# Performance work log

Measured on AMD Instinct MI355X. Metric: run time of the kernel, lower is better.

The kernel has to match this reference:

```python
import jax, jax.numpy as jnp
import numpy as np

N_NODES = 10000
W_DIM = 512
N_EDGES = 200000


def setup_inputs() -> dict:
    key = jax.random.key(0)
    k1, k2, k3 = jax.random.split(key, 3)
    z_drug = jax.random.normal(k1, (N_NODES, W_DIM), dtype=jnp.float32)
    # glorot-style init for the bilinear weight
    glorot_std = jnp.sqrt(2.0 / (W_DIM + W_DIM)).astype(jnp.float32)
    weight = jax.random.normal(k2, (W_DIM, W_DIM), dtype=jnp.float32) * glorot_std
    batch_edges = jax.random.randint(k3, (2, N_EDGES), 0, N_NODES, dtype=jnp.int64)
    return {"z_drug": z_drug, "weight": weight, "batch_edges": batch_edges}


def reference(z_drug, weight, batch_edges):
    # edge_type == 'drug_drug': both endpoints come from the drug table.
    row_embed = z_drug[batch_edges[0]]  # [E, d]
    col_embed = z_drug[batch_edges[1]]  # [E, d]
    # score_e = row_e @ W @ col_e  == diag((Z1 W) Z2^T) without the N x N blowup
    score = jnp.einsum('ed,df,ef->e', row_embed, weight, col_embed)
    return jax.nn.sigmoid(score)  # is_sigmoid=True default
```

## Files before the change

### kernel.cpp

```cpp
#include <hip/hip_runtime.h>
#include <math.h>

#define DIM     512
#define NNODES  10000
#define NEDGES  200000
#define MPAD    10240
#define NMB     160
#define GEMM_GRID (NMB * 4)
#define BKT     157

#define HIST_BLK   64
#define SCAN_BID   64
#define SCAT_BASE  65
#define SCAT_N     199
#define GEMM_BASE  264
#define FUSE_GRID  (GEMM_BASE + GEMM_GRID)
#define ECHUNK     25000

using floatx4 = __attribute__((ext_vector_type(4))) float;
using half8   = __attribute__((ext_vector_type(8))) _Float16;
using half2v  = __attribute__((ext_vector_type(2))) _Float16;
typedef unsigned long long ull;

template <int N> struct IC { static constexpr int v = N; };

__device__ inline float dot2acc(half2v a, half2v b, float c) {
#if __has_builtin(__builtin_amdgcn_fdot2)
    return __builtin_amdgcn_fdot2(a, b, c, false);
#else
    return fmaf((float)a[0], (float)b[0], fmaf((float)a[1], (float)b[1], c));
#endif
}

__device__ inline int aload(const int* p) {
    return __hip_atomic_load(p, __ATOMIC_RELAXED, __HIP_MEMORY_SCOPE_AGENT);
}
__device__ inline void astore(int* p, int v) {
    __hip_atomic_store(p, v, __ATOMIC_RELAXED, __HIP_MEMORY_SCOPE_AGENT);
}
__device__ inline void waitflag(int* f, int target) {
    while (__hip_atomic_load(f, __ATOMIC_RELAXED, __HIP_MEMORY_SCOPE_AGENT) < target)
        __builtin_amdgcn_s_sleep(8);
    __atomic_signal_fence(__ATOMIC_ACQUIRE);
}
__device__ inline void signal(int* f) {
    __atomic_signal_fence(__ATOMIC_RELEASE);
    __hip_atomic_fetch_add(f, 1, __ATOMIC_RELAXED, __HIP_MEMORY_SCOPE_AGENT);
}

#define PREP_ZBLK 2560
#define PREP_GRID (PREP_ZBLK + 64)
__global__ __launch_bounds__(256) void prep(const float* __restrict__ Z,
                                            const float* __restrict__ W,
                                            _Float16* __restrict__ Zh16,
                                            _Float16* __restrict__ Wh16t,
                                            int* __restrict__ counts) {
    const int b = blockIdx.x;
    const int t = threadIdx.x;

    if (b == 0 && t < BKT + 4) counts[t] = 0;

    if (b < PREP_ZBLK) {
        const int idx8 = (b * 256 + t) * 8;
        const int m = idx8 >> 9;
        float x[8];
        if (m < NNODES) {
            float4 v0 = *(const float4*)(Z + idx8);
            float4 v1 = *(const float4*)(Z + idx8 + 4);
            x[0]=v0.x; x[1]=v0.y; x[2]=v0.z; x[3]=v0.w;
            x[4]=v1.x; x[5]=v1.y; x[6]=v1.z; x[7]=v1.w;
        } else {
            #pragma unroll
            for (int j = 0; j < 8; ++j) x[j] = 0.f;
        }
        half8 h;
        #pragma unroll
        for (int j = 0; j < 8; ++j) h[j] = (_Float16)x[j];
        *(half8*)(Zh16 + idx8) = h;
    } else {
        __shared__ float tile[64][65];
        const int wb = b - PREP_ZBLK;
        const int kb = (wb >> 3) * 64;
        const int nb = (wb & 7) * 64;
        const int kk = t >> 2;
        const int ch = t & 3;

        const float* src = W + (size_t)(kb + kk) * DIM + nb + ch * 16;
        #pragma unroll
        for (int q = 0; q < 4; ++q) {
            float4 v = *(const float4*)(src + q * 4);
            tile[kk][ch * 16 + q * 4 + 0] = v.x;
            tile[kk][ch * 16 + q * 4 + 1] = v.y;
            tile[kk][ch * 16 + q * 4 + 2] = v.z;
            tile[kk][ch * 16 + q * 4 + 3] = v.w;
        }
        __syncthreads();

        const int nn = kk;
        half8 h0, h1;
        #pragma unroll
        for (int i = 0; i < 8; ++i) h0[i] = (_Float16)tile[ch * 16 + i][nn];
        #pragma unroll
        for (int i = 0; i < 8; ++i) h1[i] = (_Float16)tile[ch * 16 + 8 + i][nn];
        _Float16* d = Wh16t + (size_t)(nb + nn) * DIM + kb + ch * 16;
        *(half8*)(d)     = h0;
        *(half8*)(d + 8) = h1;
    }
}

__global__ __launch_bounds__(256, 3) void gemm_sort(
        const _Float16* __restrict__ Zh16,
        const _Float16* __restrict__ Wh16t,
        _Float16* __restrict__ ZWh,
        const int* __restrict__ eidx,
        int* __restrict__ counts,
        int* __restrict__ cursor,
        ull* __restrict__ slots,
        int* __restrict__ flags)
{
    __shared__ _Float16 Abuf[2][2 * 64 * 32];
    __shared__ _Float16 Bbuf[2][2 * 128 * 32];
    __shared__ int s_cnt[BKT], s_base[BKT], s_off[BKT];
    __shared__ int s_scan[256];

    const int t   = threadIdx.x;
    const int bid = blockIdx.x;

    if (bid >= GEMM_BASE) {
        const int s8  = bid - GEMM_BASE;
        const int cxd = bid & 7;
        const int rr  = s8 >> 3;
        const int mg  = (rr >> 2) * 8 + cxd;
        const int m0  = mg * 64;
        const int n0  = (rr & 3) * 128;

        const int l  = t & 63;
        const int w  = t >> 6;
        const int wn = w * 32;
        const int lm = l & 15;
        const int lq = l >> 4;
        const unsigned wbase = (unsigned)(t & 192);

        floatx4 acc[4][2] = {};

        auto stage = [&](int buf, int k0) {
            #pragma unroll
            for (int p = 0; p < 2; ++p) {
                const int s   = p * 256 + t;
                const int kk  = s >> 8;
                const int row = (s >> 2) & 63;
                const int ch  = s & 3;
                const _Float16* src = Zh16 + (size_t)(m0 + row) * DIM + k0 + kk * 32 + ch * 8;
                __builtin_amdgcn_global_load_lds(
                    (const __attribute__((address_space(1))) void*)src,
                    (__attribute__((address_space(3))) void*)&Abuf[buf][(p * 256 + wbase) * 8],
                    16, 0, 0);
            }
            #pragma unroll
            for (int p = 0; p < 4; ++p) {
                const int s   = p * 256 + t;
                const int kk  = s >> 9;
                const int row = (s >> 2) & 127;
                const int ch  = s & 3;
                const _Float16* src = Wh16t + (size_t)(n0 + row) * DIM + k0 + kk * 32 + ch * 8;
                __builtin_amdgcn_global_load_lds(
                    (const __attribute__((address_space(1))) void*)src,
                    (__attribute__((address_space(3))) void*)&Bbuf[buf][(p * 256 + wbase) * 8],
                    16, 0, 0);
            }
        };

        stage(0, 0);
        stage(1, 64);

        auto step = [&](auto Sc) {
            constexpr int S   = decltype(Sc)::v;
            constexpr int buf = S & 1;
            if constexpr (S < 7) asm volatile("s_waitcnt vmcnt(6)" ::: "memory");
            else                 asm volatile("s_waitcnt vmcnt(0)" ::: "memory");
            __builtin_amdgcn_sched_barrier(0);
            __builtin_amdgcn_s_barrier();
            __builtin_amdgcn_sched_barrier(0);

            half8 aF[2][4], bF[2][2];
            #pragma unroll
            for (int kk = 0; kk < 2; ++kk) {
                #pragma unroll
                for (int i = 0; i < 4; ++i)
                    aF[kk][i] = *(const half8*)&Abuf[buf][kk * 2048 + (16 * i + lm) * 32 + lq * 8];
                #pragma unroll
                for (int j = 0; j < 2; ++j)
                    bF[kk][j] = *(const half8*)&Bbuf[buf][kk * 4096 + (wn + 16 * j + lm) * 32 + lq * 8];
            }
            asm volatile("s_waitcnt lgkmcnt(0)" ::: "memory");
            __builtin_amdgcn_sched_barrier(0);
            __builtin_amdgcn_s_barrier();
            __builtin_amdgcn_sched_barrier(0);

            if constexpr (S < 6) stage(buf, (S + 2) * 64);

            #pragma unroll
            for (int kk = 0; kk < 2; ++kk)
                #pragma unroll
                for (int i = 0; i < 4; ++i)
                    #pragma unroll
                    for (int j = 0; j < 2; ++j)
                        acc[i][j] = __builtin_amdgcn_mfma_f32_16x16x32_f16(
                            aF[kk][i], bF[kk][j], acc[i][j], 0, 0, 0);
        };

        step(IC<0>{}); step(IC<1>{}); step(IC<2>{}); step(IC<3>{});
        step(IC<4>{}); step(IC<5>{}); step(IC<6>{}); step(IC<7>{});

        #pragma unroll
        for (int i = 0; i < 4; ++i)
            #pragma unroll
            for (int j = 0; j < 2; ++j)
                #pragma unroll
                for (int r = 0; r < 4; ++r) {
                    const int gm = m0 + 16 * i + lq * 4 + r;
                    const int gn = n0 + wn + 16 * j + lm;
                    if (gm < NNODES)
                        ZWh[(size_t)gm * DIM + gn] = (_Float16)acc[i][j][r];
                }
        return;
    }

    if (bid < HIST_BLK) {
        for (int i = t; i < BKT; i += 256) s_cnt[i] = 0;
        __syncthreads();
        for (int e = bid * 256 + t; e < NEDGES; e += HIST_BLK * 256)
            atomicAdd(&s_cnt[eidx[NEDGES + e] >> 6], 1);
        __syncthreads();
        for (int i = t; i < BKT; i += 256)
            if (s_cnt[i]) atomicAdd(&counts[i], s_cnt[i]);
        __syncthreads();
        if (t == 0) signal(&flags[0]);
        return;
    }

    if (bid == SCAN_BID) {
        if (t == 0) waitflag(&flags[0], HIST_BLK);
        __syncthreads();
        int v = (t < BKT) ? aload(counts + t) : 0;
        s_scan[t] = v;
        __syncthreads();
        #pragma unroll
        for (int off = 1; off < 256; off <<= 1) {
            int u = (t >= off) ? s_scan[t - off] : 0;
            __syncthreads();
            s_scan[t] += u;
            __syncthreads();
        }
        if (t < BKT) astore(cursor + t, s_scan[t] - v);
        __syncthreads();
        if (t == 0) signal(&flags[1]);
        return;
    }

    {
        const int sb = bid - SCAT_BASE;
        for (int i = t; i < BKT; i += 256) { s_cnt[i] = 0; s_off[i] = 0; }
        __syncthreads();
        const int e0 = sb * 1024;
        int myb[4];
        #pragma unroll
        for (int q = 0; q < 4; ++q) {
            int e = e0 + q * 256 + t;
            if (e < NEDGES) { myb[q] = eidx[NEDGES + e] >> 6; atomicAdd(&s_cnt[myb[q]], 1); }
            else myb[q] = -1;
        }
        __syncthreads();
        if (t == 0) waitflag(&flags[1], 1);
        __syncthreads();
        for (int i = t; i < BKT; i += 256)
            if (s_cnt[i]) s_base[i] = atomicAdd(&cursor[i], s_cnt[i]);
        __syncthreads();
        #pragma unroll
        for (int q = 0; q < 4; ++q)
            if (myb[q] >= 0) {
                int e = e0 + q * 256 + t;
                int r = eidx[e];
                int c = eidx[NEDGES + e];
                int pos = s_base[myb[q]] + atomicAdd(&s_off[myb[q]], 1);
                slots[pos] = ((ull)(unsigned)r << 32) |
                             (ull)(((unsigned)c << 18) | (unsigned)e);
            }
    }
}

__global__ __launch_bounds__(256) void edge_score_b(const _Float16* __restrict__ ZWh,
                                                    const _Float16* __restrict__ Zh,
                                                    const ull* __restrict__ slots,
                                                    float* __restrict__ out) {
    const int t    = threadIdx.x;
    const int lane = t & 63;
    const int gq   = lane >> 4;
    const int sl   = lane & 15;

    const int chunk = blockIdx.x & 7;
    const int blk   = blockIdx.x >> 3;
    const int ii    = chunk * ECHUNK + blk * 16 + (t >> 6) * 4 + gq;
    if (ii >= (chunk + 1) * ECHUNK) return;

    const ull  v = slots[ii];
    const unsigned k = (unsigned)v;
    const int c = (int)(k >> 18);
    const int r = (int)((v >> 32) & 0xFFFFu);

    const _Float16* rp = ZWh + (size_t)r * DIM + sl * 32;
    const _Float16* cp = Zh  + (size_t)c * DIM + sl * 32;

    half8 ra0 = *(const half8*)(rp);
    half8 ra1 = *(const half8*)(rp + 8);
    half8 ra2 = *(const half8*)(rp + 16);
    half8 ra3 = *(const half8*)(rp + 24);
    half8 c0  = *(const half8*)(cp);
    half8 c1  = *(const half8*)(cp + 8);
    half8 c2  = *(const half8*)(cp + 16);
    half8 c3  = *(const half8*)(cp + 24);

    float s = 0.f;
    #pragma unroll
    for (int d = 0; d < 4; ++d) {
        s = dot2acc((half2v){ra0[2*d], ra0[2*d+1]}, (half2v){c0[2*d], c0[2*d+1]}, s);
        s = dot2acc((half2v){ra1[2*d], ra1[2*d+1]}, (half2v){c1[2*d], c1[2*d+1]}, s);
        s = dot2acc((half2v){ra2[2*d], ra2[2*d+1]}, (half2v){c2[2*d], c2[2*d+1]}, s);
        s = dot2acc((half2v){ra3[2*d], ra3[2*d+1]}, (half2v){c3[2*d], c3[2*d+1]}, s);
    }

    s += __shfl_xor(s, 1, 64);
    s += __shfl_xor(s, 2, 64);
    s += __shfl_xor(s, 4, 64);
    s += __shfl_xor(s, 8, 64);

    if (sl == 0)
        out[k & 0x3FFFFu] = 1.0f / (1.0f + expf(-s));
}

#define GTM 128
#define GTN 64
#define GTK 16
#define LDA 132
#define LDB 68

__global__ __launch_bounds__(256) void gemm_zw(const float* __restrict__ A,
                                               const float* __restrict__ B,
                                               float* __restrict__ C) {
    __shared__ float As[GTK * LDA];
    __shared__ float Bs[GTK * LDB];

    const int t  = threadIdx.x;
    const int m0 = blockIdx.x * GTM;
    const int n0 = blockIdx.y * GTN;
    const int tx = t & 15;
    const int ty = t >> 4;

    float acc[8][4] = {};

    for (int k0 = 0; k0 < DIM; k0 += GTK) {
        #pragma unroll
        for (int p = 0; p < 2; ++p) {
            int f  = t + p * 256;
            int mm = f >> 2;
            int kq = f & 3;
            int m  = m0 + mm;
            float4 v = make_float4(0.f, 0.f, 0.f, 0.f);
            if (m < NNODES)
                v = *(const float4*)(A + (size_t)m * DIM + k0 + kq * 4);
            As[(kq * 4 + 0) * LDA + mm] = v.x;
            As[(kq * 4 + 1) * LDA + mm] = v.y;
            As[(kq * 4 + 2) * LDA + mm] = v.z;
            As[(kq * 4 + 3) * LDA + mm] = v.w;
        }
        {
            int kb = t >> 4, n4 = t & 15;
            *(float4*)&Bs[kb * LDB + n4 * 4] =
                *(const float4*)(B + (size_t)(k0 + kb) * DIM + n0 + n4 * 4);
        }
        __syncthreads();

        #pragma unroll
        for (int kk = 0; kk < GTK; ++kk) {
            float4 a0 = *(const float4*)&As[kk * LDA + ty * 8];
            float4 a1 = *(const float4*)&As[kk * LDA + ty * 8 + 4];
            float4 b  = *(const float4*)&Bs[kk * LDB + tx * 4];
            float av[8] = {a0.x, a0.y, a0.z, a0.w, a1.x, a1.y, a1.z, a1.w};
            float bv[4] = {b.x, b.y, b.z, b.w};
            #pragma unroll
            for (int i = 0; i < 8; ++i)
                #pragma unroll
                for (int j = 0; j < 4; ++j)
                    acc[i][j] = fmaf(av[i], bv[j], acc[i][j]);
        }
        __syncthreads();
    }

    #pragma unroll
    for (int i = 0; i < 8; ++i) {
        int m = m0 + ty * 8 + i;
        if (m < NNODES)
            *(float4*)(C + (size_t)m * DIM + n0 + tx * 4) =
                make_float4(acc[i][0], acc[i][1], acc[i][2], acc[i][3]);
    }
}

__global__ __launch_bounds__(256) void edge_score(const float* __restrict__ ZW,
                                                  const float* __restrict__ Z,
                                                  const int* __restrict__ eidx,
                                                  float* __restrict__ out) {
    const int e    = blockIdx.x * 4 + (threadIdx.x >> 6);
    const int lane = threadIdx.x & 63;

    const int r = eidx[e];
    const int c = eidx[NEDGES + e];

    const float4* pr = (const float4*)(ZW + (size_t)r * DIM);
    const float4* pc = (const float4*)(Z  + (size_t)c * DIM);

    float4 a0 = pr[lane * 2 + 0];
    float4 a1 = pr[lane * 2 + 1];
    float4 b0 = pc[lane * 2 + 0];
    float4 b1 = pc[lane * 2 + 1];

    float s = a0.x * b0.x;
    s = fmaf(a0.y, b0.y, s);
    s = fmaf(a0.z, b0.z, s);
    s = fmaf(a0.w, b0.w, s);
    s = fmaf(a1.x, b1.x, s);
    s = fmaf(a1.y, b1.y, s);
    s = fmaf(a1.z, b1.z, s);
    s = fmaf(a1.w, b1.w, s);

    #pragma unroll
    for (int off = 32; off > 0; off >>= 1)
        s += __shfl_xor(s, off, 64);

    if (lane == 0)
        out[e] = 1.0f / (1.0f + expf(-s));
}

extern "C" void kernel_launch(void* const* d_in, const int* in_sizes, int n_in,
                              void* d_out, int out_size, void* d_ws, size_t ws_size,
                              hipStream_t stream) {
    const float* Z  = (const float*)d_in[0];
    const float* W  = (const float*)d_in[1];
    const int*   EI = (const int*)d_in[2];
    float* out = (float*)d_out;

    char* p = (char*)d_ws;
    _Float16* ZWh   = (_Float16*)p;  p += (size_t)MPAD * DIM * 2;
    _Float16* Zh16  = (_Float16*)p;  p += (size_t)MPAD * DIM * 2;
    _Float16* Wh16t = (_Float16*)p;  p += (size_t)DIM * DIM * 2;
    int* counts  = (int*)p;          p += (size_t)BKT * 4;
    int* flags   = (int*)p;          p += 4 * 4;
    int* cursor  = (int*)p;          p += (size_t)BKT * 4;
    ull* slots   = (ull*)p;          p += (size_t)NEDGES * 8;
    const size_t need_full = (size_t)(p - (char*)d_ws);

    if (ws_size >= need_full) {
        prep<<<PREP_GRID, 256, 0, stream>>>(Z, W, Zh16, Wh16t, counts);
        gemm_sort<<<FUSE_GRID, 256, 0, stream>>>(Zh16, Wh16t, ZWh, EI, counts,
                                                 cursor, slots, flags);
        edge_score_b<<<8 * ((ECHUNK + 15) / 16), 256, 0, stream>>>(ZWh, Zh16, slots, out);
    } else {
        float* ZW = (float*)d_ws;
        dim3 g1((NNODES + GTM - 1) / GTM, DIM / GTN);
        gemm_zw<<<g1, 256, 0, stream>>>(Z, W, ZW);
        edge_score<<<NEDGES / 4, 256, 0, stream>>>(ZW, Z, EI, out);
    }
}
```

Baseline: 132.2 us.

## Fuse edge scoring into GEMM epilogue using LDS-resident ZW tiles and row-sorted edges

The edge-scoring kernel is removed. Each GEMM block now keeps its 64x128 ZW tile in LDS as fp32 and, once the scatter blocks signal, walks the edges whose row falls in its 64-row bucket. It accumulates partial dot products over its 128-column slice into a global score buffer with atomicAdd, and a small final kernel applies the sigmoid. Edges are now bucketed by row instead of column. This avoids writing the full ZW matrix to global memory and gathering it back per edge. The cost is four atomic adds per edge, GEMM blocks spinning on scatter completion while holding CU slots, and a dependence on cross-block flag ordering.

```diff
diff --git a/kernel.cpp b/kernel.cpp
--- a/kernel.cpp
+++ b/kernel.cpp
@@ -9,13 +9,13 @@
 #define GEMM_GRID (NMB * 4)
 #define BKT     157
 
+#define GEMM_N     640
+#define HIST_BASE  640
 #define HIST_BLK   64
-#define SCAN_BID   64
-#define SCAT_BASE  65
+#define SCAN_BID   704
+#define SCAT_BASE  705
 #define SCAT_N     199
-#define GEMM_BASE  264
-#define FUSE_GRID  (GEMM_BASE + GEMM_GRID)
-#define ECHUNK     25000
+#define FUSE_GRID  904
 
 using floatx4 = __attribute__((ext_vector_type(4))) float;
 using half8   = __attribute__((ext_vector_type(8))) _Float16;
@@ -43,9 +43,17 @@
         __builtin_amdgcn_s_sleep(8);
     __atomic_signal_fence(__ATOMIC_ACQUIRE);
 }
+__device__ inline void waitflag_acq(int* f, int target) {
+    while (__hip_atomic_load(f, __ATOMIC_RELAXED, __HIP_MEMORY_SCOPE_AGENT) < target)
+        __builtin_amdgcn_s_sleep(8);
+    (void)__hip_atomic_load(f, __ATOMIC_ACQUIRE, __HIP_MEMORY_SCOPE_AGENT);
+}
 __device__ inline void signal(int* f) {
     __atomic_signal_fence(__ATOMIC_RELEASE);
     __hip_atomic_fetch_add(f, 1, __ATOMIC_RELAXED, __HIP_MEMORY_SCOPE_AGENT);
+}
+__device__ inline void signal_rel(int* f) {
+    __hip_atomic_fetch_add(f, 1, __ATOMIC_RELEASE, __HIP_MEMORY_SCOPE_AGENT);
 }
 
 #define PREP_ZBLK 2560
@@ -54,11 +62,17 @@
                                             const float* __restrict__ W,
                                             _Float16* __restrict__ Zh16,
                                             _Float16* __restrict__ Wh16t,
-                                            int* __restrict__ counts) {
+                                            int* __restrict__ counts,
+                                            float* __restrict__ score_acc) {
     const int b = blockIdx.x;
     const int t = threadIdx.x;
 
     if (b == 0 && t < BKT + 4) counts[t] = 0;
+    if (b < 196) {
+        int i = b * 256 + t;
+        if (i < NEDGES / 4)
+            ((float4*)score_acc)[i] = make_float4(0.f, 0.f, 0.f, 0.f);
+    }
 
     if (b < PREP_ZBLK) {
         const int idx8 = (b * 256 + t) * 8;
@@ -108,28 +122,30 @@
     }
 }
 
+#define ZWL_LD 132
 __global__ __launch_bounds__(256, 3) void gemm_sort(
         const _Float16* __restrict__ Zh16,
         const _Float16* __restrict__ Wh16t,
-        _Float16* __restrict__ ZWh,
         const int* __restrict__ eidx,
         int* __restrict__ counts,
         int* __restrict__ cursor,
         ull* __restrict__ slots,
+        float* __restrict__ score_acc,
         int* __restrict__ flags)
 {
-    __shared__ _Float16 Abuf[2][2 * 64 * 32];
-    __shared__ _Float16 Bbuf[2][2 * 128 * 32];
+    __shared__ __align__(16) char smem[49152];
+    _Float16 (*Abuf)[2 * 64 * 32]  = reinterpret_cast<_Float16(*)[2 * 64 * 32]>(smem);
+    _Float16 (*Bbuf)[2 * 128 * 32] = reinterpret_cast<_Float16(*)[2 * 128 * 32]>(smem + 16384);
+    float* ZWl = reinterpret_cast<float*>(smem);
     __shared__ int s_cnt[BKT], s_base[BKT], s_off[BKT];
     __shared__ int s_scan[256];
 
     const int t   = threadIdx.x;
     const int bid = blockIdx.x;
 
-    if (bid >= GEMM_BASE) {
-        const int s8  = bid - GEMM_BASE;
+    if (bid < GEMM_N) {
         const int cxd = bid & 7;
-        const int rr  = s8 >> 3;
+        const int rr  = bid >> 3;
         const int mg  = (rr >> 2) * 8 + cxd;
         const int m0  = mg * 64;
         const int n0  = (rr & 3) * 128;
@@ -212,25 +228,64 @@
         step(IC<0>{}); step(IC<1>{}); step(IC<2>{}); step(IC<3>{});
         step(IC<4>{}); step(IC<5>{}); step(IC<6>{}); step(IC<7>{});
 
+        if (mg >= BKT) return;
+
+        __syncthreads();
         #pragma unroll
         for (int i = 0; i < 4; ++i)
             #pragma unroll
             for (int j = 0; j < 2; ++j)
                 #pragma unroll
-                for (int r = 0; r < 4; ++r) {
-                    const int gm = m0 + 16 * i + lq * 4 + r;
-                    const int gn = n0 + wn + 16 * j + lm;
-                    if (gm < NNODES)
-                        ZWh[(size_t)gm * DIM + gn] = (_Float16)acc[i][j][r];
-                }
+                for (int r = 0; r < 4; ++r)
+                    ZWl[(16 * i + lq * 4 + r) * ZWL_LD + wn + 16 * j + lm] = acc[i][j][r];
+        __syncthreads();
+
+        if (t == 0) waitflag_acq(&flags[2], SCAT_N);
+        __syncthreads();
+
+        const int end   = aload(cursor + mg);
+        const int start = mg ? aload(cursor + mg - 1) : 0;
+        const int gq = l >> 4;
+        const int sl = l & 15;
+
+        for (int base = start; base < end; base += 16) {
+            const int idx = base + w * 4 + gq;
+            float s = 0.f;
+            int e = -1;
+            if (idx < end) {
+                const ull v = slots[idx];
+                e = (int)(v & 0x3FFFFu);
+                const int c  = (int)((v >> 18) & 0x3FFFu);
+                const int rl = (int)(v >> 32) - m0;
+                const float* zw = ZWl + rl * ZWL_LD + sl * 8;
+                const half8 cv = *(const half8*)(Zh16 + (size_t)c * DIM + n0 + sl * 8);
+                const float4 z0 = *(const float4*)(zw);
+                const float4 z1 = *(const float4*)(zw + 4);
+                s = fmaf(z0.x, (float)cv[0], s);
+                s = fmaf(z0.y, (float)cv[1], s);
+                s = fmaf(z0.z, (float)cv[2], s);
+                s = fmaf(z0.w, (float)cv[3], s);
+                s = fmaf(z1.x, (float)cv[4], s);
+                s = fmaf(z1.y, (float)cv[5], s);
+                s = fmaf(z1.z, (float)cv[6], s);
+                s = fmaf(z1.w, (float)cv[7], s);
+            }
+            s += __shfl_xor(s, 1, 64);
+            s += __shfl_xor(s, 2, 64);
+            s += __shfl_xor(s, 4, 64);
+            s += __shfl_xor(s, 8, 64);
+            if (sl == 0 && e >= 0 && e < NEDGES)
+                atomicAdd(score_acc + e, s);
+        }
         return;
     }
 
-    if (bid < HIST_BLK) {
+    if (bid < SCAN_BID) {
+        const int hb = bid - HIST_BASE;
         for (int i = t; i < BKT; i += 256) s_cnt[i] = 0;
         __syncthreads();
-        for (int e = bid * 256 + t; e < NEDGES; e += HIST_BLK * 256)
-            atomicAdd(&s_cnt[eidx[NEDGES + e] >> 6], 1);
+        for (int e = hb * 256 + t; e < NEDGES; e += HIST_BLK * 256)
+            atomicAdd(&s_cnt[eidx[e] >> 6], 1);
         __syncthreads();
         for (int i = t; i < BKT; i += 256)
             if (s_cnt[i]) atomicAdd(&counts[i], s_cnt[i]);
@@ -267,7 +322,7 @@
         #pragma unroll
         for (int q = 0; q < 4; ++q) {
             int e = e0 + q * 256 + t;
-            if (e < NEDGES) { myb[q] = eidx[NEDGES + e] >> 6; atomicAdd(&s_cnt[myb[q]], 1); }
+            if (e < NEDGES) { myb[q] = eidx[e] >> 6; atomicAdd(&s_cnt[myb[q]], 1); }
             else myb[q] = -1;
         }
         __syncthreads();
@@ -286,56 +341,23 @@
                 slots[pos] = ((ull)(unsigned)r << 32) |
                              (ull)(((unsigned)c << 18) | (unsigned)e);
             }
-    }
-}
-
-__global__ __launch_bounds__(256) void edge_score_b(const _Float16* __restrict__ ZWh,
-                                                    const _Float16* __restrict__ Zh,
-                                                    const ull* __restrict__ slots,
-                                                    float* __restrict__ out) {
-    const int t    = threadIdx.x;
-    const int lane = t & 63;
-    const int gq   = lane >> 4;
-    const int sl   = lane & 15;
-
-    const int chunk = blockIdx.x & 7;
-    const int blk   = blockIdx.x >> 3;
-    const int ii    = chunk * ECHUNK + blk * 16 + (t >> 6) * 4 + gq;
-    if (ii >= (chunk + 1) * ECHUNK) return;
-
-    const ull  v = slots[ii];
-    const unsigned k = (unsigned)v;
-    const int c = (int)(k >> 18);
-    const int r = (int)((v >> 32) & 0xFFFFu);
-
-    const _Float16* rp = ZWh + (size_t)r * DIM + sl * 32;
-    const _Float16* cp = Zh  + (size_t)c * DIM + sl * 32;
-
-    half8 ra0 = *(const half8*)(rp);
-    half8 ra1 = *(const half8*)(rp + 8);
-    half8 ra2 = *(const half8*)(rp + 16);
-    half8 ra3 = *(const half8*)(rp + 24);
-    half8 c0  = *(const half8*)(cp);
-    half8 c1  = *(const half8*)(cp + 8);
-    half8 c2  = *(const half8*)(cp + 16);
-    half8 c3  = *(const half8*)(cp + 24);
-
-    float s = 0.f;
-    #pragma unroll
-    for (int d = 0; d < 4; ++d) {
-        s = dot2acc((half2v){ra0[2*d], ra0[2*d+1]}, (half2v){c0[2*d], c0[2*d+1]}, s);
-        s = dot2acc((half2v){ra1[2*d], ra1[2*d+1]}, (half2v){c1[2*d], c1[2*d+1]}, s);
-        s = dot2acc((half2v){ra2[2*d], ra2[2*d+1]}, (half2v){c2[2*d], c2[2*d+1]}, s);
-        s = dot2acc((half2v){ra3[2*d], ra3[2*d+1]}, (half2v){c3[2*d], c3[2*d+1]}, s);
-    }
-
-    s += __shfl_xor(s, 1, 64);
-    s += __shfl_xor(s, 2, 64);
-    s += __shfl_xor(s, 4, 64);
-    s += __shfl_xor(s, 8, 64);
-
-    if (sl == 0)
-        out[k & 0x3FFFFu] = 1.0f / (1.0f + expf(-s));
+        __syncthreads();
+        if (t == 0) signal_rel(&flags[2]);
+    }
+}
+
+__global__ __launch_bounds__(256) void sigmoid_out(const float* __restrict__ acc,
+                                                   float* __restrict__ out) {
+    const int i = blockIdx.x * 256 + threadIdx.x;
+    if (i < NEDGES / 4) {
+        float4 v = ((const float4*)acc)[i];
+        float4 o;
+        o.x = 1.0f / (1.0f + expf(-v.x));
+        o.y = 1.0f / (1.0f + expf(-v.y));
+        o.z = 1.0f / (1.0f + expf(-v.z));
+        o.w = 1.0f / (1.0f + expf(-v.w));
+        ((float4*)out)[i] = o;
+    }
 }
 
 #define GTM 128
@@ -449,20 +471,20 @@
     float* out = (float*)d_out;
 
     char* p = (char*)d_ws;
-    _Float16* ZWh   = (_Float16*)p;  p += (size_t)MPAD * DIM * 2;
     _Float16* Zh16  = (_Float16*)p;  p += (size_t)MPAD * DIM * 2;
     _Float16* Wh16t = (_Float16*)p;  p += (size_t)DIM * DIM * 2;
     int* counts  = (int*)p;          p += (size_t)BKT * 4;
     int* flags   = (int*)p;          p += 4 * 4;
     int* cursor  = (int*)p;          p += (size_t)BKT * 4;
     ull* slots   = (ull*)p;          p += (size_t)NEDGES * 8;
+    float* score_acc = (float*)p;    p += (size_t)NEDGES * 4;
     const size_t need_full = (size_t)(p - (char*)d_ws);
 
     if (ws_size >= need_full) {
-        prep<<<PREP_GRID, 256, 0, stream>>>(Z, W, Zh16, Wh16t, counts);
-        gemm_sort<<<FUSE_GRID, 256, 0, stream>>>(Zh16, Wh16t, ZWh, EI, counts,
-                                                 cursor, slots, flags);
-        edge_score_b<<<8 * ((ECHUNK + 15) / 16), 256, 0, stream>>>(ZWh, Zh16, slots, out);
+        prep<<<PREP_GRID, 256, 0, stream>>>(Z, W, Zh16, Wh16t, counts, score_acc);
+        gemm_sort<<<FUSE_GRID, 256, 0, stream>>>(Zh16, Wh16t, EI, counts,
+                                                 cursor, slots, score_acc, flags);
+        sigmoid_out<<<(NEDGES / 4 + 255) / 256, 256, 0, stream>>>(score_acc, out);
     } else {
         float* ZW = (float*)d_ws;
         dim3 g1((NNODES + GTM - 1) / GTM, DIM / GTN);
```

Result: slower. 218.5 us (+65.3%).
